# Kernel optimization log

Measured on AMD Instinct MI355X. Metric: run time of the kernel, lower is better.

Reference implementation:

```python
import jax, jax.numpy as jnp
import numpy as np

COMMITMENT_FACTOR = 0.25
QUANTIZATION_FACTOR = 1.0


def setup_inputs() -> dict:
    key = jax.random.key(0)
    k1, k2 = jax.random.split(key)
    B, D, H, W = 64, 256, 32, 32
    K = 1024
    z = jax.random.normal(k1, (B, D, H, W), dtype=jnp.float32)
    # torch init: uniform(-1/K, 1/K)
    codebook = jax.random.uniform(k2, (K, D), dtype=jnp.float32,
                                  minval=-1.0 / K, maxval=1.0 / K)
    return {"z": z, "codebook": codebook}


def reference(z, codebook):
    # z: [B, D, H, W]; codebook: [K, D]
    B, D, H, W = z.shape
    z_nhwc = jnp.transpose(z, (0, 2, 3, 1))          # [B, H, W, D]
    z_flat = z_nhwc.reshape(-1, D)                    # [N, D]
    # squared euclidean distances: ||z||^2 + ||w||^2 - 2 z.w
    dist = (jnp.sum(z_flat ** 2, axis=-1, keepdims=True)
            + jnp.sum(codebook ** 2, axis=-1)
            - 2.0 * z_flat @ codebook.T)              # [N, K]
    closest = jnp.argmin(dist, axis=-1)               # [N]
    quantized_indices = closest.reshape(B, H, W)
    # one-hot @ codebook == gather
    q_flat = codebook[closest]                        # [N, D]
    quantized = q_flat.reshape(B, H, W, D)

    commitment_loss = jnp.sum((jax.lax.stop_gradient(quantized) - z_nhwc) ** 2)
    embedding_loss = jnp.sum((quantized - jax.lax.stop_gradient(z_nhwc)) ** 2)
    loss = commitment_loss * COMMITMENT_FACTOR + embedding_loss * QUANTIZATION_FACTOR

    # straight-through estimator
    quantized_st = z_nhwc + jax.lax.stop_gradient(quantized - z_nhwc)
    quantized_st = jnp.transpose(quantized_st, (0, 3, 1, 2))  # [B, D, H, W]
    quantized_indices = quantized_indices[:, None, :, :]       # [B, 1, H, W]
    return quantized_st, quantized_indices, loss
```

## Files before the change

### kernel.cpp

```cpp
#include <hip/hip_runtime.h>


#define IDX_OFF  16777216
#define LOSS_OFF 16842752

typedef __bf16 bf16x8 __attribute__((ext_vector_type(8)));
typedef float  f32x4  __attribute__((ext_vector_type(4)));

__global__ __launch_bounds__(256) void vq_prep(const float* __restrict__ cb,
                                               __bf16* __restrict__ cbh,
                                               __bf16* __restrict__ cbf,
                                               float* __restrict__ sc1) {
    const int t = threadIdx.x;
    const int r = blockIdx.x * 16 + (t >> 4);
    const int d0 = (t & 15) * 16;
    const float* src = cb + (size_t)r * 256 + d0;
    __bf16* dst = cbh + (size_t)r * 256 + d0;
    float s = 0.f;
    float4 f[4];
    #pragma unroll
    for (int p = 0; p < 4; p++) f[p] = *(const float4*)(src + p * 4);
    bf16x8 v0, v1;
    #pragma unroll
    for (int p = 0; p < 4; p++) {
        s = fmaf(f[p].x, f[p].x, s); s = fmaf(f[p].y, f[p].y, s);
        s = fmaf(f[p].z, f[p].z, s); s = fmaf(f[p].w, f[p].w, s);
    }
    v0[0]=(__bf16)f[0].x; v0[1]=(__bf16)f[0].y; v0[2]=(__bf16)f[0].z; v0[3]=(__bf16)f[0].w;
    v0[4]=(__bf16)f[1].x; v0[5]=(__bf16)f[1].y; v0[6]=(__bf16)f[1].z; v0[7]=(__bf16)f[1].w;
    v1[0]=(__bf16)f[2].x; v1[1]=(__bf16)f[2].y; v1[2]=(__bf16)f[2].z; v1[3]=(__bf16)f[2].w;
    v1[4]=(__bf16)f[3].x; v1[5]=(__bf16)f[3].y; v1[6]=(__bf16)f[3].z; v1[7]=(__bf16)f[3].w;
    *(bf16x8*)dst = v0;
    *(bf16x8*)(dst + 8) = v1;
    {
        const int slot = ((r >> 4) * 8 + (d0 >> 5)) * 512 + ((r & 15) * 4 + ((d0 >> 3) & 3)) * 8;
        *(bf16x8*)&cbf[slot]     = v0;
        *(bf16x8*)&cbf[slot + 8] = v1;
    }
    s += __shfl_xor(s, 1, 64);
    s += __shfl_xor(s, 2, 64);
    s += __shfl_xor(s, 4, 64);
    s += __shfl_xor(s, 8, 64);
    if ((t & 15) == 0) sc1[r] = s + 1.0f;
}

__global__ __launch_bounds__(256, 2) void vq_mfma(const float* __restrict__ z,
                                                  const __bf16* __restrict__ cbh,
                                                  const __bf16* __restrict__ cbf,
                                                  const float* __restrict__ sc1,
                                                  float* __restrict__ out) {
    __shared__ __align__(16) __bf16 z_s[64 * 256];
    __shared__ float red_s[4];

    const int t    = threadIdx.x;
    const int lane = t & 63;
    const int w    = t >> 6;
    const int m16  = lane & 15;
    const int q4   = lane >> 4;
    const int wc   = w << 6;
    const int lidx = m16 * 4 + q4;
    const int blk  = blockIdx.x;
    const int b    = blk >> 4;
    const int hw0  = (blk & 15) << 6;
    const int n0   = blk << 6;
    const int kt0  = (blk & 3) << 8;

    bf16x8 bb[4];
    {
        const __bf16* bp = cbf + (size_t)((kt0 + wc) >> 4) * 4096 + lidx * 8;
        #pragma unroll
        for (int j = 0; j < 4; j++) bb[j] = *(const bf16x8*)(bp + (size_t)j * 4096);
    }

    float lz = 0.f;
    {
        const int rg    = (t & 15) * 4;
        const int dbase = (t >> 4) * 16;
        const float* zp = z + (size_t)b * 262144 + hw0 + rg;
        #pragma unroll
        for (int batch = 0; batch < 2; batch++) {
            float4 f[8];
            #pragma unroll
            for (int j = 0; j < 8; j++)
                f[j] = *(const float4*)(zp + (size_t)(dbase + batch * 8 + j) * 1024);
            const float* fp = (const float*)f;
            #pragma unroll
            for (int r = 0; r < 4; r++) {
                bf16x8 v;
                #pragma unroll
                for (int j = 0; j < 8; j++) {
                    float x = fp[j * 4 + r];
                    lz = fmaf(x, x, lz);
                    v[j] = (__bf16)x;
                }
                const int row = rg + r;
                const int gs  = ((t >> 4) * 2 + batch) ^ (row & 7);
                *(bf16x8*)&z_s[row * 256 + gs * 8] = v;
            }
        }
    }
    __syncthreads();

    unsigned int best[16];
    #pragma unroll
    for (int i = 0; i < 16; i++) best[i] = 0xFFFFFFFFu;

    #pragma unroll 1
    for (int it = 0; it < 4; it++) {
        const int kt  = (kt0 + (it << 8)) & 1023;
        const int ktn = (kt0 + (((it + 1) & 3) << 8)) & 1023;
        int   kcv[4];
        float sck[4];
        #pragma unroll
        for (int j = 0; j < 4; j++) {
            kcv[j] = kt + wc + j * 16 + m16;
            sck[j] = sc1[kcv[j]];
        }
        const __bf16* bt  = cbf + (size_t)((kt  + wc) >> 4) * 4096 + lidx * 8;
        const __bf16* btn = cbf + (size_t)((ktn + wc) >> 4) * 4096 + lidx * 8;

        f32x4 acc[4][4];
        #pragma unroll
        for (int i = 0; i < 4; i++)
            #pragma unroll
            for (int j = 0; j < 4; j++) acc[i][j] = (f32x4){0.f, 0.f, 0.f, 0.f};

        #pragma unroll
        for (int dcs = 0; dcs < 8; dcs++) {
            bf16x8 bn[4];
            const __bf16* bp = (dcs < 7) ? (bt + (dcs + 1) * 512) : btn;
            #pragma unroll
            for (int j = 0; j < 4; j++) bn[j] = *(const bf16x8*)(bp + (size_t)j * 4096);

            const int gs = (dcs * 4 + q4) ^ (m16 & 7);
            #pragma unroll
            for (int i = 0; i < 4; i++) {
                bf16x8 a = *(const bf16x8*)&z_s[(i * 16 + m16) * 256 + gs * 8];
                #pragma unroll
                for (int j = 0; j < 4; j++)
                    acc[i][j] = __builtin_amdgcn_mfma_f32_16x16x32_bf16(a, bb[j], acc[i][j], 0, 0, 0);
            }

            #pragma unroll
            for (int j = 0; j < 4; j++) bb[j] = bn[j];
        }

        #pragma unroll
        for (int j = 0; j < 4; j++) {
            #pragma unroll
            for (int i = 0; i < 4; i++)
                #pragma unroll
                for (int r = 0; r < 4; r++) {
                    float v3 = fmaf(-2.f, acc[i][j][r], sck[j]);
                    unsigned int key = (__float_as_uint(v3) & 0xFFFFFC00u) | (unsigned int)kcv[j];
                    int pos = i * 4 + r;
                    best[pos] = min(best[pos], key);
                }
        }
    }

    #pragma unroll
    for (int pos = 0; pos < 16; pos++) {
        unsigned int k = best[pos];
        #pragma unroll
        for (int off = 1; off < 16; off <<= 1)
            k = min(k, (unsigned int)__shfl_xor((int)k, off, 64));
        best[pos] = k;
    }
    __syncthreads();

    unsigned int* ks = (unsigned int*)z_s;
    if (m16 == 0) {
        #pragma unroll
        for (int pos = 0; pos < 16; pos++) {
            int i = pos >> 2, r = pos & 3;
            int row = i * 16 + q4 * 4 + r;
            ks[w * 64 + row] = best[pos];
        }
    }
    __syncthreads();
    if (t < 64) {
        unsigned int key = min(min(ks[t], ks[64 + t]), min(ks[128 + t], ks[192 + t]));
        int kf = (int)(key & 1023u);
        ks[256 + t] = (unsigned int)kf;
        out[IDX_OFF + n0 + t] = (float)kf;
        lz += __uint_as_float(key & 0xFFFFFC00u) - 1.0f;
    }
    {
        float s = lz;
        #pragma unroll
        for (int off = 1; off < 64; off <<= 1) s += __shfl_xor(s, off, 64);
        if (lane == 0) red_s[w] = s;
    }
    __syncthreads();
    if (t == 0)
        atomicAdd(out + LOSS_OFF, 1.25f * ((red_s[0] + red_s[1]) + (red_s[2] + red_s[3])));

    const int qrow = t >> 2;
    const int qoff = (t & 3) * 64;
    const int myk  = (int)ks[256 + qrow];
    __syncthreads();
    {
        const __bf16* qp = cbh + (size_t)myk * 256 + qoff;
        #pragma unroll
        for (int p = 0; p < 8; p++) {
            bf16x8 v = *(const bf16x8*)(qp + p * 8);
            int gs = ((qoff >> 3) + p) ^ (qrow & 7);
            *(bf16x8*)&z_s[qrow * 256 + gs * 8] = v;
        }
    }
    __syncthreads();
    {
        const int nl   = t & 63;
        const int dseg = t >> 6;
        float* op = out + (size_t)(b * 256 + dseg * 64) * 1024 + hw0 + nl;
        #pragma unroll
        for (int p = 0; p < 8; p++) {
            int gs = (dseg * 8 + p) ^ (nl & 7);
            bf16x8 v = *(const bf16x8*)&z_s[nl * 256 + gs * 8];
            #pragma unroll
            for (int j = 0; j < 8; j++)
                op[(size_t)(p * 8 + j) * 1024] = (float)v[j];
        }
    }
}

extern "C" void kernel_launch(void* const* d_in, const int* in_sizes, int n_in,
                              void* d_out, int out_size, void* d_ws, size_t ws_size,
                              hipStream_t stream) {
    const float* z  = (const float*)d_in[0];
    const float* cb = (const float*)d_in[1];
    float* out = (float*)d_out;

    float*  sc1 = (float*)d_ws;
    __bf16* cbh = (__bf16*)((char*)d_ws + 8192);
    __bf16* cbf = (__bf16*)((char*)d_ws + 8192 + 524288);

    hipMemsetAsync(out + LOSS_OFF, 0, sizeof(float), stream);
    vq_prep<<<64, 256, 0, stream>>>(cb, cbh, cbf, sc1);
    vq_mfma<<<1024, 256, 0, stream>>>(z, cbh, cbf, sc1, out);
}
```

Baseline: 187.7 us.

## Retile waves as 2x2 over rows and codes with deeper B-fragment prefetch

Changes the per-wave work split from all 64 rows by 64 codes to 32 rows by 64 codes, with the two wave pairs covering 128 codes per iteration over 8 iterations instead of 4. Codebook fragments are now prefetched three d-chunks ahead in a register ring, and the A fragments from LDS are double-buffered one step ahead. This aims to hide global/L2 latency on the codebook loads and to cut accumulator register pressure, which could allow better scheduling. In exchange each A fragment is reused across fewer MFMAs and the codebook is loaded twice per block, doubling codebook load traffic.

```diff
diff --git a/kernel.cpp b/kernel.cpp
--- a/kernel.cpp
+++ b/kernel.cpp
@@ -57,7 +57,8 @@
     const int w    = t >> 6;
     const int m16  = lane & 15;
     const int q4   = lane >> 4;
-    const int wc   = w << 6;
+    const int wn   = (w >> 1) * 32;
+    const int wk   = (w & 1) * 64;
     const int lidx = m16 * 4 + q4;
     const int blk  = blockIdx.x;
     const int b    = blk >> 4;
@@ -65,11 +66,14 @@
     const int n0   = blk << 6;
     const int kt0  = (blk & 3) << 8;
 
-    bf16x8 bb[4];
-    {
-        const __bf16* bp = cbf + (size_t)((kt0 + wc) >> 4) * 4096 + lidx * 8;
-        #pragma unroll
-        for (int j = 0; j < 4; j++) bb[j] = *(const bf16x8*)(bp + (size_t)j * 4096);
+    bf16x8 bq[3][4];
+    {
+        const __bf16* bp = cbf + (size_t)((kt0 + wk) >> 4) * 4096 + lidx * 8;
+        #pragma unroll
+        for (int s = 0; s < 3; s++)
+            #pragma unroll
+            for (int j = 0; j < 4; j++)
+                bq[s][j] = *(const bf16x8*)(bp + (size_t)j * 4096 + s * 512);
     }
 
     float lz = 0.f;
@@ -101,54 +105,73 @@
     }
     __syncthreads();
 
-    unsigned int best[16];
-    #pragma unroll
-    for (int i = 0; i < 16; i++) best[i] = 0xFFFFFFFFu;
+    unsigned int best[8];
+    #pragma unroll
+    for (int i = 0; i < 8; i++) best[i] = 0xFFFFFFFFu;
+
+    bf16x8 a0[2];
+    {
+        const int gs = q4 ^ (m16 & 7);
+        #pragma unroll
+        for (int i = 0; i < 2; i++)
+            a0[i] = *(const bf16x8*)&z_s[(wn + i * 16 + m16) * 256 + gs * 8];
+    }
 
     #pragma unroll 1
-    for (int it = 0; it < 4; it++) {
-        const int kt  = (kt0 + (it << 8)) & 1023;
-        const int ktn = (kt0 + (((it + 1) & 3) << 8)) & 1023;
+    for (int it = 0; it < 8; it++) {
+        const int kt  = (kt0 + (it << 7)) & 1023;
+        const int ktn = (kt0 + (((it + 1) & 7) << 7)) & 1023;
         int   kcv[4];
         float sck[4];
         #pragma unroll
         for (int j = 0; j < 4; j++) {
-            kcv[j] = kt + wc + j * 16 + m16;
+            kcv[j] = kt + wk + j * 16 + m16;
             sck[j] = sc1[kcv[j]];
         }
-        const __bf16* bt  = cbf + (size_t)((kt  + wc) >> 4) * 4096 + lidx * 8;
-        const __bf16* btn = cbf + (size_t)((ktn + wc) >> 4) * 4096 + lidx * 8;
-
-        f32x4 acc[4][4];
-        #pragma unroll
-        for (int i = 0; i < 4; i++)
+        const __bf16* bt  = cbf + (size_t)((kt  + wk) >> 4) * 4096 + lidx * 8;
+        const __bf16* btn = cbf + (size_t)((ktn + wk) >> 4) * 4096 + lidx * 8;
+
+        f32x4 acc[2][4];
+        #pragma unroll
+        for (int i = 0; i < 2; i++)
             #pragma unroll
             for (int j = 0; j < 4; j++) acc[i][j] = (f32x4){0.f, 0.f, 0.f, 0.f};
 
         #pragma unroll
         for (int dcs = 0; dcs < 8; dcs++) {
             bf16x8 bn[4];
-            const __bf16* bp = (dcs < 7) ? (bt + (dcs + 1) * 512) : btn;
-            #pragma unroll
-            for (int j = 0; j < 4; j++) bn[j] = *(const bf16x8*)(bp + (size_t)j * 4096);
-
-            const int gs = (dcs * 4 + q4) ^ (m16 & 7);
-            #pragma unroll
-            for (int i = 0; i < 4; i++) {
-                bf16x8 a = *(const bf16x8*)&z_s[(i * 16 + m16) * 256 + gs * 8];
+            {
+                const __bf16* bp = (dcs < 5) ? (bt + (dcs + 3) * 512) : (btn + (dcs - 5) * 512);
+                #pragma unroll
+                for (int j = 0; j < 4; j++) bn[j] = *(const bf16x8*)(bp + (size_t)j * 4096);
+            }
+            bf16x8 an[2];
+            {
+                const int gsn = ((((dcs + 1) & 7) * 4) + q4) ^ (m16 & 7);
+                #pragma unroll
+                for (int i = 0; i < 2; i++)
+                    an[i] = *(const bf16x8*)&z_s[(wn + i * 16 + m16) * 256 + gsn * 8];
+            }
+
+            #pragma unroll
+            for (int i = 0; i < 2; i++)
                 #pragma unroll
                 for (int j = 0; j < 4; j++)
-                    acc[i][j] = __builtin_amdgcn_mfma_f32_16x16x32_bf16(a, bb[j], acc[i][j], 0, 0, 0);
-            }
-
-            #pragma unroll
-            for (int j = 0; j < 4; j++) bb[j] = bn[j];
+                    acc[i][j] = __builtin_amdgcn_mfma_f32_16x16x32_bf16(a0[i], bq[0][j], acc[i][j], 0, 0, 0);
+
+            a0[0] = an[0]; a0[1] = an[1];
+            #pragma unroll
+            for (int j = 0; j < 4; j++) {
+                bq[0][j] = bq[1][j];
+                bq[1][j] = bq[2][j];
+                bq[2][j] = bn[j];
+            }
         }
 
         #pragma unroll
         for (int j = 0; j < 4; j++) {
             #pragma unroll
-            for (int i = 0; i < 4; i++)
+            for (int i = 0; i < 2; i++)
                 #pragma unroll
                 for (int r = 0; r < 4; r++) {
                     float v3 = fmaf(-2.f, acc[i][j][r], sck[j]);
@@ -160,7 +183,7 @@
     }
 
     #pragma unroll
-    for (int pos = 0; pos < 16; pos++) {
+    for (int pos = 0; pos < 8; pos++) {
         unsigned int k = best[pos];
         #pragma unroll
         for (int off = 1; off < 16; off <<= 1)
@@ -172,15 +195,15 @@
     unsigned int* ks = (unsigned int*)z_s;
     if (m16 == 0) {
         #pragma unroll
-        for (int pos = 0; pos < 16; pos++) {
+        for (int pos = 0; pos < 8; pos++) {
             int i = pos >> 2, r = pos & 3;
-            int row = i * 16 + q4 * 4 + r;
-            ks[w * 64 + row] = best[pos];
+            int row = wn + i * 16 + q4 * 4 + r;
+            ks[(w & 1) * 64 + row] = best[pos];
         }
     }
     __syncthreads();
     if (t < 64) {
-        unsigned int key = min(min(ks[t], ks[64 + t]), min(ks[128 + t], ks[192 + t]));
+        unsigned int key = min(ks[t], ks[64 + t]);
         int kf = (int)(key & 1023u);
         ks[256 + t] = (unsigned int)kf;
         out[IDX_OFF + n0 + t] = (float)kf;
```

Measured after the change: 180.7 us. 1.04x faster.
